# Kernel optimization log

Measured on AMD Instinct MI355X. Metric: run time of the kernel, lower is better.

Reference implementation:

```python
import jax, jax.numpy as jnp
import numpy as np
import math

D = 1024
B, S = 8, 2048


def setup_inputs() -> dict:
    key = jax.random.key(0)
    ks = jax.random.split(key, 8)
    q = jax.random.normal(ks[0], (B, S, D), dtype=jnp.float32)
    k = jax.random.normal(ks[1], (B, S, D), dtype=jnp.float32)
    v1 = jax.random.normal(ks[2], (B, S, D), dtype=jnp.float32)
    mask = jax.random.normal(ks[3], (1, S, S), dtype=jnp.float32)
    # Linear params: torch Linear stores W as [out, in]; init ~ U(-1/sqrt(in), 1/sqrt(in))
    lim = 1.0 / math.sqrt(D)
    W1 = jax.random.uniform(ks[4], (D, D), jnp.float32, -lim, lim)
    b1 = jax.random.uniform(ks[5], (D,), jnp.float32, -lim, lim)
    W2 = jax.random.uniform(ks[6], (D, D), jnp.float32, -lim, lim)
    b2 = jax.random.uniform(ks[7], (D,), jnp.float32, -lim, lim)
    return {"q": q, "k": k, "v1": v1, "mask": mask,
            "W1": W1, "b1": b1, "W2": W2, "b2": b2}


def _proj(x, W1, b1, W2, b2):
    # linear2(linear1(x)); torch Linear: x @ W.T + b
    h = jnp.einsum('bsd,od->bso', x, W1) + b1
    return jnp.einsum('bsd,od->bso', h, W2) + b2


def reference(q, k, v1, mask, W1, b1, W2, b2):
    qp = _proj(q, W1, b1, W2, b2)          # [B,S,D]
    kp = _proj(k, W1, b1, W2, b2)          # [B,S,D]
    scale = 1.0 / math.sqrt(qp.shape[-1])
    qk = jnp.einsum('bqd,bkd->bqk', qp, kp) * scale  # [B,S,S]
    qk = qk + mask                          # broadcast [1,S,S]
    attn = jax.nn.softmax(qk, axis=-1)
    return jnp.einsum('bqk,bkd->bqd', attn, v1)  # [B,S,D]
```

## Files before the change

### kernel.cpp

```cpp
#include <hip/hip_runtime.h>
#include <hip/hip_bf16.h>

typedef __hip_bfloat16 bf16;
typedef __bf16 bf16x8 __attribute__((ext_vector_type(8)));
typedef float f32x4 __attribute__((ext_vector_type(4)));

constexpr int Bn = 8, Sn = 2048, Dn = 1024;
constexpr int BM = 128, BN = 128, BK = 64;

__global__ void cast2_f32_bf16_k(const float* __restrict__ x0, const float* __restrict__ x1,
                                 bf16* __restrict__ y, int n ) {
  int i = (blockIdx.x * blockDim.x + threadIdx.x) * 4;
  const float* src = (i < n) ? (x0 + i) : (x1 + (i - n));
  float4 f = *reinterpret_cast<const float4*>(src);
  bf16 tmp[4] = {__float2bfloat16(f.x), __float2bfloat16(f.y),
                 __float2bfloat16(f.z), __float2bfloat16(f.w)};
  *reinterpret_cast<short4*>(y + i) = *reinterpret_cast<const short4*>(tmp);
}

__global__ void cast_f32_bf16_k(const float* __restrict__ x, bf16* __restrict__ y, int n) {
  int i = (blockIdx.x * blockDim.x + threadIdx.x) * 4;
  if (i >= n) return;
  float4 f = *reinterpret_cast<const float4*>(x + i);
  bf16 tmp[4] = {__float2bfloat16(f.x), __float2bfloat16(f.y),
                 __float2bfloat16(f.z), __float2bfloat16(f.w)};
  *reinterpret_cast<short4*>(y + i) = *reinterpret_cast<const short4*>(tmp);
}

__global__ void transpose_cast_k(const float* __restrict__ src0, bf16* __restrict__ dst0,
                                 int R, int C) {
  __shared__ float tile[32][33];
  const int r0 = blockIdx.x * 32, c0 = blockIdx.y * 32, b = blockIdx.z;
  const float* src = src0 + (size_t)b * R * C;
  bf16* dst = dst0 + (size_t)b * C * R;
  const int tx = threadIdx.x & 31, ty = threadIdx.x >> 5;
  #pragma unroll
  for (int i = 0; i < 4; ++i) {
    int r = ty + i * 8;
    tile[r][tx] = src[(size_t)(r0 + r) * C + c0 + tx];
  }
  __syncthreads();
  #pragma unroll
  for (int i = 0; i < 4; ++i) {
    int c = ty + i * 8;
    dst[(size_t)(c0 + c) * R + r0 + tx] = __float2bfloat16(tile[tx][c]);
  }
}

__global__ __launch_bounds__(256)
void bias_compose_k(const float* __restrict__ W2, const float* __restrict__ b1,
                    const float* __restrict__ b2, float* __restrict__ bc) {
  const int row = blockIdx.x;
  const int t = threadIdx.x;
  float4 wv = *reinterpret_cast<const float4*>(W2 + (size_t)row * Dn + t * 4);
  float4 bv = *reinterpret_cast<const float4*>(b1 + t * 4);
  float s = wv.x * bv.x + wv.y * bv.y + wv.z * bv.z + wv.w * bv.w;
  #pragma unroll
  for (int off = 32; off >= 1; off >>= 1) s += __shfl_xor(s, off);
  __shared__ float ssum[4];
  if ((t & 63) == 0) ssum[t >> 6] = s;
  __syncthreads();
  if (t == 0) bc[row] = (ssum[0] + ssum[1]) + (ssum[2] + ssum[3]) + b2[row];
}

#define SBAR()  asm volatile("s_barrier" ::: "memory")
#define LGKM0() asm volatile("s_waitcnt lgkmcnt(0)" ::: "memory")
#define VM0()   asm volatile("s_waitcnt vmcnt(0)" ::: "memory")

#define MFMA16() do {                                                         \
    __builtin_amdgcn_s_setprio(1);                                            \
    _Pragma("unroll")                                                         \
    for (int kk = 0; kk < 2; ++kk)                                            \
      _Pragma("unroll")                                                       \
      for (int mi4 = 0; mi4 < 4; ++mi4)                                       \
        _Pragma("unroll")                                                     \
        for (int n2 = 0; n2 < 2; ++n2)                                        \
          acc[mi4][n2] = __builtin_amdgcn_mfma_f32_16x16x32_bf16(             \
              aF[mi4][kk], bF[n2][kk], acc[mi4][n2], 0, 0, 0);                \
    __builtin_amdgcn_s_setprio(0);                                            \
  } while (0)

#define ITER(cur, T) do {                                                     \
    const bool pf = (T) + 1 < NT;                                             \
    if (pf) {                                                                 \
      stage2((1 - (cur)) * 32768,         Abase, (T) + 1);                    \
      stage2((1 - (cur)) * 32768 + 16384, Bbase, (T) + 1);                    \
    }                                                                         \
    _Pragma("unroll")                                                         \
    for (int mi4 = 0; mi4 < 4; ++mi4) {                                       \
      aF[mi4][0] = *reinterpret_cast<const bf16x8*>(pA0 + (cur)*32768 + mi4*2048); \
      aF[mi4][1] = *reinterpret_cast<const bf16x8*>(pA1 + (cur)*32768 + mi4*2048); \
    }                                                                         \
    _Pragma("unroll")                                                         \
    for (int j = 0; j < 2; ++j) {                                             \
      bF[j][0] = *reinterpret_cast<const bf16x8*>(pB0 + (cur)*32768 + j*2048); \
      bF[j][1] = *reinterpret_cast<const bf16x8*>(pB1 + (cur)*32768 + j*2048); \
    }                                                                         \
    LGKM0();                                                                  \
    MFMA16();                                                                 \
    if (pf) VM0();                                                            \
    SBAR();                                                                   \
  } while (0)

template<int EPI>
__global__ __launch_bounds__(512, 4)
void gemm128_k(const bf16* __restrict__ A, const bf16* __restrict__ BT,
               void* __restrict__ Cv, const float* __restrict__ aux,
               int N, int K, long long sAz, long long sBz, long long sCz,
               float scale, int gx, int gy)
{
  __shared__ __align__(128) bf16 sh[2 * 16384];

  const int nwg = (int)gridDim.x;
  const int flat = (int)blockIdx.x;
  const int swz = (flat & 7) * (nwg >> 3) + (flat >> 3);
  const int tn = swz % gx;
  const int rem = swz / gx;
  const int tm = rem % gy;
  const int z  = rem / gy;

  const int t = threadIdx.x, w = t >> 6, lane = t & 63;
  const int wm = w >> 2, wn = w & 3;
  const int fr = lane & 15, kg = lane >> 4;
  const int m0 = tm * BM, n0 = tn * BN;
  const bf16* Abase = A + (size_t)z * sAz + (size_t)m0 * K;
  const bf16* Bbase = BT + (size_t)z * sBz + (size_t)n0 * K;

  f32x4 acc[4][2];
  const f32x4 fz = {0.f, 0.f, 0.f, 0.f};
  #pragma unroll
  for (int i = 0; i < 4; ++i) { acc[i][0] = fz; acc[i][1] = fz; }
  bf16x8 aF[4][2], bF[2][2];

  const char* shB = (const char*)sh;
  const int swzlo = (fr & 3) << 4;
  const int swzhi = (fr & 4) << 4;
  const int aoff0 = (wm * 64 + fr) * 128 + ((kg * 16) ^ swzlo) + swzhi;
  const int boff0 = 16384 + (wn * 32 + fr) * 128 + ((kg * 16) ^ swzlo) + swzhi;
  const char* pA0 = shB + aoff0;
  const char* pA1 = shB + (aoff0 ^ 64);
  const char* pB0 = shB + boff0;
  const char* pB1 = shB + (boff0 ^ 64);

  int gOff[2];
  #pragma unroll
  for (int i = 0; i < 2; ++i) {
    const int slot = i * 512 + w * 64 + lane;
    const int row = slot >> 3;
    const int cb = (slot & 7) ^ (row & 7);
    gOff[i] = row * K + cb * 8;
  }
  auto stage2 = [&](int dstByte, const bf16* gbase, int kt) {
    const bf16* g0 = gbase + (size_t)kt * BK;
    char* db = (char*)sh + dstByte;
    #pragma unroll
    for (int i = 0; i < 2; ++i) {
      __builtin_amdgcn_global_load_lds(
          (__attribute__((address_space(1))) void*)(g0 + gOff[i]),
          (__attribute__((address_space(3))) void*)(db + (i * 512 + w * 64) * 16),
          16, 0, 0);
    }
  };

  const int NT = K / BK;
  stage2(0,     Abase, 0);
  stage2(16384, Bbase, 0);
  VM0();
  SBAR();

  for (int T = 0; T < NT; T += 2) {
    ITER(0, T);
    ITER(1, T + 1);
  }

  const int or0 = kg * 4;
  if constexpr (EPI == 0) {
    bf16* C = (bf16*)Cv + (size_t)z * sCz;
    #pragma unroll
    for (int mi = 0; mi < 4; ++mi)
      #pragma unroll
      for (int r = 0; r < 4; ++r) {
        const int row = m0 + wm * 64 + mi * 16 + or0 + r;
        #pragma unroll
        for (int nj = 0; nj < 2; ++nj) {
          const int col = n0 + wn * 32 + nj * 16 + fr;
          C[(size_t)row * N + col] = __float2bfloat16(acc[mi][nj][r] + aux[col]);
        }
      }
  } else if constexpr (EPI == 1) {
    bf16* C = (bf16*)Cv + (size_t)z * sCz;
    #pragma unroll
    for (int mi = 0; mi < 4; ++mi)
      #pragma unroll
      for (int r = 0; r < 4; ++r) {
        const int row = m0 + wm * 64 + mi * 16 + or0 + r;
        #pragma unroll
        for (int nj = 0; nj < 2; ++nj) {
          const int col = n0 + wn * 32 + nj * 16 + fr;
          float v = __expf(acc[mi][nj][r] * scale + aux[(size_t)row * N + col]);
          C[(size_t)row * N + col] = __float2bfloat16(v);
        }
      }
  } else if constexpr (EPI == 2) {
    float* C = (float*)Cv + (size_t)z * sCz;
    const float* Zb = aux + (size_t)z * Sn;
    #pragma unroll
    for (int mi = 0; mi < 4; ++mi)
      #pragma unroll
      for (int r = 0; r < 4; ++r) {
        const int row = m0 + wm * 64 + mi * 16 + or0 + r;
        const float invZ = 1.0f / Zb[row];
        #pragma unroll
        for (int nj = 0; nj < 2; ++nj) {
          const int col = n0 + wn * 32 + nj * 16 + fr;
          C[(size_t)row * N + col] = acc[mi][nj][r] * invZ;
        }
      }
  } else {
    bf16* C = (bf16*)Cv + (size_t)z * sCz;
    #pragma unroll
    for (int mi = 0; mi < 4; ++mi)
      #pragma unroll
      for (int r = 0; r < 4; ++r) {
        const int row = m0 + wm * 64 + mi * 16 + or0 + r;
        #pragma unroll
        for (int nj = 0; nj < 2; ++nj) {
          const int col = n0 + wn * 32 + nj * 16 + fr;
          C[(size_t)row * N + col] = __float2bfloat16(acc[mi][nj][r]);
        }
      }
  }
}

__global__ __launch_bounds__(256)
void rowsum_k(const bf16* __restrict__ sc, float* __restrict__ Z) {
  const size_t row = blockIdx.x;
  const bf16* p = sc + row * (size_t)Sn;
  const int t = threadIdx.x;
  unsigned short raw[8];
  *reinterpret_cast<int4*>(raw) = *reinterpret_cast<const int4*>(p + t * 8);
  float s = 0.f;
  #pragma unroll
  for (int j = 0; j < 8; ++j) s += __uint_as_float(((unsigned)raw[j]) << 16);
  #pragma unroll
  for (int off = 32; off >= 1; off >>= 1) s += __shfl_xor(s, off);
  __shared__ float ssum[4];
  if ((t & 63) == 0) ssum[t >> 6] = s;
  __syncthreads();
  if (t == 0) Z[row] = (ssum[0] + ssum[1]) + (ssum[2] + ssum[3]);
}

extern "C" void kernel_launch(void* const* d_in, const int* in_sizes, int n_in,
                              void* d_out, int out_size, void* d_ws, size_t ws_size,
                              hipStream_t stream) {
  const float* q    = (const float*)d_in[0];
  const float* k    = (const float*)d_in[1];
  const float* v1   = (const float*)d_in[2];
  const float* mask = (const float*)d_in[3];
  const float* W1   = (const float*)d_in[4];
  const float* b1   = (const float*)d_in[5];
  const float* W2   = (const float*)d_in[6];
  const float* b2   = (const float*)d_in[7];
  float* out = (float*)d_out;

  const size_t nQKD = (size_t)Bn * Sn * Dn;
  char* ws = (char*)d_ws;
  bf16* qkb  = (bf16*)ws;
  bf16* vtb  = qkb + 2 * nQKD;
  bf16* hb   = vtb + nQKD;
  bf16* w1t  = hb + 2 * nQKD;
  bf16* w2b  = w1t + (size_t)Dn * Dn;
  bf16* wcb  = w2b + (size_t)Dn * Dn;
  bf16* scb  = wcb + (size_t)Dn * Dn;
  float* Zb  = (float*)(scb + (size_t)Bn * Sn * Sn);
  float* bcb = Zb + (size_t)Bn * Sn;

  dim3 blk(256);
  const int nQK = (int)nQKD;
  cast2_f32_bf16_k<<<dim3(2 * nQK / 4 / 256), blk, 0, stream>>>(q, k, qkb, nQK);
  cast_f32_bf16_k<<<dim3(Dn * Dn / 4 / 256), blk, 0, stream>>>(W2, w2b, Dn * Dn);
  transpose_cast_k<<<dim3(Dn / 32, Dn / 32, 1), blk, 0, stream>>>(W1, w1t, Dn, Dn);
  transpose_cast_k<<<dim3(Sn / 32, Dn / 32, Bn), blk, 0, stream>>>(v1, vtb, Sn, Dn);
  bias_compose_k<<<dim3(Dn), blk, 0, stream>>>(W2, b1, b2, bcb);

  const int M2 = 2 * Bn * Sn;
  dim3 gblk(512);
  gemm128_k<3><<<dim3(8 * 8), gblk, 0, stream>>>(
      w2b, w1t, wcb, nullptr, Dn, Dn, 0, 0, 0, 1.f, 8, 8);
  gemm128_k<0><<<dim3(8 * (M2 / 128)), gblk, 0, stream>>>(
      qkb, wcb, hb, bcb, Dn, Dn, 0, 0, 0, 1.f, 8, M2 / 128);
  gemm128_k<1><<<dim3(16 * 16 * Bn), gblk, 0, stream>>>(
      hb, hb + nQKD, scb, mask, Sn, Dn,
      (long long)Sn * Dn, (long long)Sn * Dn, (long long)Sn * Sn, 0.03125f, 16, 16);
  rowsum_k<<<dim3(Bn * Sn), blk, 0, stream>>>(scb, Zb);
  gemm128_k<2><<<dim3(8 * 16 * Bn), gblk, 0, stream>>>(
      scb, vtb, out, Zb, Dn, Sn,
      (long long)Sn * Sn, (long long)Dn * Sn, (long long)Sn * Dn, 1.f, 8, 16);
}
```

Baseline: 341.3 us.

## Fuse fp32-to-bf16 cast of q/k into projection GEMM A-loads; bf16 mask

Removes the separate cast kernel for q and k. The projection GEMM now loads fp32 A tiles into registers, converts them to bf16 and writes them to LDS itself, which saves one write and read of 2×B×S×D bf16 in global memory. The mask is pre-cast to bf16 once, so the score epilogue reads half the bytes. In exchange, A staging now goes through registers instead of direct global-to-LDS loads, adding register pressure and an extra LDS-write wait per iteration, and the mask loses precision.

```diff
diff --git a/kernel.cpp b/kernel.cpp
--- a/kernel.cpp
+++ b/kernel.cpp
@@ -7,16 +7,6 @@
 
 constexpr int Bn = 8, Sn = 2048, Dn = 1024;
 constexpr int BM = 128, BN = 128, BK = 64;
-
-__global__ void cast2_f32_bf16_k(const float* __restrict__ x0, const float* __restrict__ x1,
-                                 bf16* __restrict__ y, int n ) {
-  int i = (blockIdx.x * blockDim.x + threadIdx.x) * 4;
-  const float* src = (i < n) ? (x0 + i) : (x1 + (i - n));
-  float4 f = *reinterpret_cast<const float4*>(src);
-  bf16 tmp[4] = {__float2bfloat16(f.x), __float2bfloat16(f.y),
-                 __float2bfloat16(f.z), __float2bfloat16(f.w)};
-  *reinterpret_cast<short4*>(y + i) = *reinterpret_cast<const short4*>(tmp);
-}
 
 __global__ void cast_f32_bf16_k(const float* __restrict__ x, bf16* __restrict__ y, int n) {
   int i = (blockIdx.x * blockDim.x + threadIdx.x) * 4;
@@ -82,8 +72,17 @@
 
 #define ITER(cur, T) do {                                                     \
     const bool pf = (T) + 1 < NT;                                             \
+    float4 a0, a1, a2, a3;                                                    \
     if (pf) {                                                                 \
-      stage2((1 - (cur)) * 32768,         Abase, (T) + 1);                    \
+      if constexpr (AF32) {                                                   \
+        const float* gf = Af + (size_t)((T) + 1) * BK;                        \
+        a0 = *reinterpret_cast<const float4*>(gf + gOffF[0]);                 \
+        a1 = *reinterpret_cast<const float4*>(gf + gOffF[0] + 4);             \
+        a2 = *reinterpret_cast<const float4*>(gf + gOffF[1]);                 \
+        a3 = *reinterpret_cast<const float4*>(gf + gOffF[1] + 4);             \
+      } else {                                                                \
+        stage2((1 - (cur)) * 32768, Abase, (T) + 1);                          \
+      }                                                                       \
       stage2((1 - (cur)) * 32768 + 16384, Bbase, (T) + 1);                    \
     }                                                                         \
     _Pragma("unroll")                                                         \
@@ -98,14 +97,22 @@
     }                                                                         \
     LGKM0();                                                                  \
     MFMA16();                                                                 \
-    if (pf) VM0();                                                            \
+    if (pf) {                                                                 \
+      VM0();                                                                  \
+      if constexpr (AF32) {                                                   \
+        wrA((1 - (cur)) * 32768, a0, a1, a2, a3);                             \
+        LGKM0();                                                              \
+      }                                                                       \
+    }                                                                         \
     SBAR();                                                                   \
   } while (0)
 
-template<int EPI>
+template<int EPI, bool AF32>
 __global__ __launch_bounds__(512, 4)
-void gemm128_k(const bf16* __restrict__ A, const bf16* __restrict__ BT,
-               void* __restrict__ Cv, const float* __restrict__ aux,
+void gemm128_k(const bf16* __restrict__ A,
+               const float* __restrict__ Aq, const float* __restrict__ Ak, int rowSplit,
+               const bf16* __restrict__ BT,
+               void* __restrict__ Cv, const void* __restrict__ auxv,
                int N, int K, long long sAz, long long sBz, long long sCz,
                float scale, int gx, int gy)
 {
@@ -125,6 +132,9 @@
   const int m0 = tm * BM, n0 = tn * BN;
   const bf16* Abase = A + (size_t)z * sAz + (size_t)m0 * K;
   const bf16* Bbase = BT + (size_t)z * sBz + (size_t)n0 * K;
+  const float* Af = nullptr;
+  if constexpr (AF32)
+    Af = (m0 < rowSplit) ? Aq + (size_t)m0 * K : Ak + (size_t)(m0 - rowSplit) * K;
 
   f32x4 acc[4][2];
   const f32x4 fz = {0.f, 0.f, 0.f, 0.f};
@@ -142,13 +152,14 @@
   const char* pB0 = shB + boff0;
   const char* pB1 = shB + (boff0 ^ 64);
 
-  int gOff[2];
+  int gOff[2], gOffF[2];
   #pragma unroll
   for (int i = 0; i < 2; ++i) {
     const int slot = i * 512 + w * 64 + lane;
     const int row = slot >> 3;
     const int cb = (slot & 7) ^ (row & 7);
-    gOff[i] = row * K + cb * 8;
+    gOff[i]  = row * K + cb * 8;
+    gOffF[i] = row * K + cb * 8;
   }
   auto stage2 = [&](int dstByte, const bf16* gbase, int kt) {
     const bf16* g0 = gbase + (size_t)kt * BK;
@@ -161,12 +172,31 @@
           16, 0, 0);
     }
   };
+  auto wrA = [&](int dstByte, float4 x0, float4 x1, float4 x2, float4 x3) {
+    char* db = (char*)sh + dstByte;
+    bf16 tmp[16] = {
+      __float2bfloat16(x0.x), __float2bfloat16(x0.y), __float2bfloat16(x0.z), __float2bfloat16(x0.w),
+      __float2bfloat16(x1.x), __float2bfloat16(x1.y), __float2bfloat16(x1.z), __float2bfloat16(x1.w),
+      __float2bfloat16(x2.x), __float2bfloat16(x2.y), __float2bfloat16(x2.z), __float2bfloat16(x2.w),
+      __float2bfloat16(x3.x), __float2bfloat16(x3.y), __float2bfloat16(x3.z), __float2bfloat16(x3.w)};
+    *reinterpret_cast<int4*>(db + (0 * 512 + t) * 16) = *reinterpret_cast<const int4*>(tmp);
+    *reinterpret_cast<int4*>(db + (1 * 512 + t) * 16) = *reinterpret_cast<const int4*>(tmp + 8);
+  };
 
   const int NT = K / BK;
-  stage2(0,     Abase, 0);
-  stage2(16384, Bbase, 0);
-  VM0();
-  SBAR();
+  if constexpr (AF32) {
+    float4 a0 = *reinterpret_cast<const float4*>(Af + gOffF[0]);
+    float4 a1 = *reinterpret_cast<const float4*>(Af + gOffF[0] + 4);
+    float4 a2 = *reinterpret_cast<const float4*>(Af + gOffF[1]);
+    float4 a3 = *reinterpret_cast<const float4*>(Af + gOffF[1] + 4);
+    stage2(16384, Bbase, 0);
+    wrA(0, a0, a1, a2, a3);
+    VM0(); LGKM0(); SBAR();
+  } else {
+    stage2(0,     Abase, 0);
+    stage2(16384, Bbase, 0);
+    VM0(); SBAR();
+  }
 
   for (int T = 0; T < NT; T += 2) {
     ITER(0, T);
@@ -176,6 +206,7 @@
   const int or0 = kg * 4;
   if constexpr (EPI == 0) {
     bf16* C = (bf16*)Cv + (size_t)z * sCz;
+    const float* aux = (const float*)auxv;
     #pragma unroll
     for (int mi = 0; mi < 4; ++mi)
       #pragma unroll
@@ -189,6 +220,7 @@
       }
   } else if constexpr (EPI == 1) {
     bf16* C = (bf16*)Cv + (size_t)z * sCz;
+    const bf16* M = (const bf16*)auxv;
     #pragma unroll
     for (int mi = 0; mi < 4; ++mi)
       #pragma unroll
@@ -197,13 +229,14 @@
         #pragma unroll
         for (int nj = 0; nj < 2; ++nj) {
           const int col = n0 + wn * 32 + nj * 16 + fr;
-          float v = __expf(acc[mi][nj][r] * scale + aux[(size_t)row * N + col]);
+          float mv = __bfloat162float(M[(size_t)row * N + col]);
+          float v = __expf(acc[mi][nj][r] * scale + mv);
           C[(size_t)row * N + col] = __float2bfloat16(v);
         }
       }
   } else if constexpr (EPI == 2) {
     float* C = (float*)Cv + (size_t)z * sCz;
-    const float* Zb = aux + (size_t)z * Sn;
+    const float* Zb = (const float*)auxv + (size_t)z * Sn;
     #pragma unroll
     for (int mi = 0; mi < 4; ++mi)
       #pragma unroll
@@ -265,35 +298,34 @@
 
   const size_t nQKD = (size_t)Bn * Sn * Dn;
   char* ws = (char*)d_ws;
-  bf16* qkb  = (bf16*)ws;
-  bf16* vtb  = qkb + 2 * nQKD;
-  bf16* hb   = vtb + nQKD;
-  bf16* w1t  = hb + 2 * nQKD;
-  bf16* w2b  = w1t + (size_t)Dn * Dn;
-  bf16* wcb  = w2b + (size_t)Dn * Dn;
-  bf16* scb  = wcb + (size_t)Dn * Dn;
-  float* Zb  = (float*)(scb + (size_t)Bn * Sn * Sn);
-  float* bcb = Zb + (size_t)Bn * Sn;
+  bf16* vtb   = (bf16*)ws;
+  bf16* hb    = vtb + nQKD;
+  bf16* w1t   = hb + 2 * nQKD;
+  bf16* w2b   = w1t + (size_t)Dn * Dn;
+  bf16* wcb   = w2b + (size_t)Dn * Dn;
+  bf16* maskb = wcb + (size_t)Dn * Dn;
+  bf16* scb   = maskb + (size_t)Sn * Sn;
+  float* Zb   = (float*)(scb + (size_t)Bn * Sn * Sn);
+  float* bcb  = Zb + (size_t)Bn * Sn;
 
   dim3 blk(256);
-  const int nQK = (int)nQKD;
-  cast2_f32_bf16_k<<<dim3(2 * nQK / 4 / 256), blk, 0, stream>>>(q, k, qkb, nQK);
   cast_f32_bf16_k<<<dim3(Dn * Dn / 4 / 256), blk, 0, stream>>>(W2, w2b, Dn * Dn);
+  cast_f32_bf16_k<<<dim3(Sn * Sn / 4 / 256), blk, 0, stream>>>(mask, maskb, Sn * Sn);
   transpose_cast_k<<<dim3(Dn / 32, Dn / 32, 1), blk, 0, stream>>>(W1, w1t, Dn, Dn);
   transpose_cast_k<<<dim3(Sn / 32, Dn / 32, Bn), blk, 0, stream>>>(v1, vtb, Sn, Dn);
   bias_compose_k<<<dim3(Dn), blk, 0, stream>>>(W2, b1, b2, bcb);
 
   const int M2 = 2 * Bn * Sn;
   dim3 gblk(512);
-  gemm128_k<3><<<dim3(8 * 8), gblk, 0, stream>>>(
-      w2b, w1t, wcb, nullptr, Dn, Dn, 0, 0, 0, 1.f, 8, 8);
-  gemm128_k<0><<<dim3(8 * (M2 / 128)), gblk, 0, stream>>>(
-      qkb, wcb, hb, bcb, Dn, Dn, 0, 0, 0, 1.f, 8, M2 / 128);
-  gemm128_k<1><<<dim3(16 * 16 * Bn), gblk, 0, stream>>>(
-      hb, hb + nQKD, scb, mask, Sn, Dn,
+  gemm128_k<3, false><<<dim3(8 * 8), gblk, 0, stream>>>(
+      w2b, nullptr, nullptr, 0, w1t, wcb, nullptr, Dn, Dn, 0, 0, 0, 1.f, 8, 8);
+  gemm128_k<0, true><<<dim3(8 * (M2 / 128)), gblk, 0, stream>>>(
+      nullptr, q, k, Bn * Sn, wcb, hb, bcb, Dn, Dn, 0, 0, 0, 1.f, 8, M2 / 128);
+  gemm128_k<1, false><<<dim3(16 * 16 * Bn), gblk, 0, stream>>>(
+      hb, nullptr, nullptr, 0, hb + nQKD, scb, maskb, Sn, Dn,
       (long long)Sn * Dn, (long long)Sn * Dn, (long long)Sn * Sn, 0.03125f, 16, 16);
   rowsum_k<<<dim3(Bn * Sn), blk, 0, stream>>>(scb, Zb);
-  gemm128_k<2><<<dim3(8 * 16 * Bn), gblk, 0, stream>>>(
-      scb, vtb, out, Zb, Dn, Sn,
+  gemm128_k<2, false><<<dim3(8 * 16 * Bn), gblk, 0, stream>>>(
+      scb, nullptr, nullptr, 0, vtb, out, Zb, Dn, Sn,
       (long long)Sn * Sn, (long long)Dn * Sn, (long long)Sn * Dn, 1.f, 8, 16);
 }
```

Result: slower. 406.5 us (+19.1%).

## Fold the composed projection into a Gram matrix so only K is projected

Applied to the files above, without the earlier changes.

Rewrites the scores algebraically as q·(Wcᵀ Wc)·kᵀ plus rank-one bias terms. It precomputes the Gram matrix G and the vectors u = Wcᵀbc and c0 = bc·bc, and stops projecting q. Only k goes through the large projection GEMM, and the bias contributions are added in the score epilogue as per-row and per-column scalars. The q/k fp32→bf16 cast is fused with the dot products against u, which adds a few small kernels. The extra bf16 rounding of G and the row-constant term folded into the unshifted exp could shift numerics slightly.

```diff
diff --git a/kernel.cpp b/kernel.cpp
--- a/kernel.cpp
+++ b/kernel.cpp
@@ -7,16 +7,6 @@
 
 constexpr int Bn = 8, Sn = 2048, Dn = 1024;
 constexpr int BM = 128, BN = 128, BK = 64;
-
-__global__ void cast2_f32_bf16_k(const float* __restrict__ x0, const float* __restrict__ x1,
-                                 bf16* __restrict__ y, int n ) {
-  int i = (blockIdx.x * blockDim.x + threadIdx.x) * 4;
-  const float* src = (i < n) ? (x0 + i) : (x1 + (i - n));
-  float4 f = *reinterpret_cast<const float4*>(src);
-  bf16 tmp[4] = {__float2bfloat16(f.x), __float2bfloat16(f.y),
-                 __float2bfloat16(f.z), __float2bfloat16(f.w)};
-  *reinterpret_cast<short4*>(y + i) = *reinterpret_cast<const short4*>(tmp);
-}
 
 __global__ void cast_f32_bf16_k(const float* __restrict__ x, bf16* __restrict__ y, int n) {
   int i = (blockIdx.x * blockDim.x + threadIdx.x) * 4;
@@ -61,6 +51,64 @@
   if ((t & 63) == 0) ssum[t >> 6] = s;
   __syncthreads();
   if (t == 0) bc[row] = (ssum[0] + ssum[1]) + (ssum[2] + ssum[3]) + b2[row];
+}
+
+__global__ __launch_bounds__(256)
+void udot_k(const bf16* __restrict__ wct, const float* __restrict__ bc,
+            float* __restrict__ u) {
+  const int i = blockIdx.x, t = threadIdx.x;
+  short4 wv = *reinterpret_cast<const short4*>(wct + (size_t)i * Dn + t * 4);
+  float4 bv = *reinterpret_cast<const float4*>(bc + t * 4);
+  float s = __uint_as_float(((unsigned)(unsigned short)wv.x) << 16) * bv.x
+          + __uint_as_float(((unsigned)(unsigned short)wv.y) << 16) * bv.y
+          + __uint_as_float(((unsigned)(unsigned short)wv.z) << 16) * bv.z
+          + __uint_as_float(((unsigned)(unsigned short)wv.w) << 16) * bv.w;
+  #pragma unroll
+  for (int off = 32; off >= 1; off >>= 1) s += __shfl_xor(s, off);
+  __shared__ float ssum[4];
+  if ((t & 63) == 0) ssum[t >> 6] = s;
+  __syncthreads();
+  if (t == 0) u[i] = (ssum[0] + ssum[1]) + (ssum[2] + ssum[3]);
+}
+
+__global__ __launch_bounds__(256)
+void c0_k(const float* __restrict__ bc, float* __restrict__ c0) {
+  const int t = threadIdx.x;
+  float4 bv = *reinterpret_cast<const float4*>(bc + t * 4);
+  float s = bv.x * bv.x + bv.y * bv.y + bv.z * bv.z + bv.w * bv.w;
+  #pragma unroll
+  for (int off = 32; off >= 1; off >>= 1) s += __shfl_xor(s, off);
+  __shared__ float ssum[4];
+  if ((t & 63) == 0) ssum[t >> 6] = s;
+  __syncthreads();
+  if (t == 0) c0[0] = (ssum[0] + ssum[1]) + (ssum[2] + ssum[3]);
+}
+
+__global__ __launch_bounds__(256)
+void castdot_k(const float* __restrict__ q, const float* __restrict__ k,
+               const float* __restrict__ u, const float* __restrict__ c0,
+               bf16* __restrict__ dst, float* __restrict__ qu, float* __restrict__ ku) {
+  const int row = blockIdx.x;
+  const bool isQ = row < Bn * Sn;
+  const float* src = isQ ? q + (size_t)row * Dn : k + (size_t)(row - Bn * Sn) * Dn;
+  const int t = threadIdx.x;
+  float4 f = *reinterpret_cast<const float4*>(src + t * 4);
+  bf16 tmp[4] = {__float2bfloat16(f.x), __float2bfloat16(f.y),
+                 __float2bfloat16(f.z), __float2bfloat16(f.w)};
+  *reinterpret_cast<short4*>(dst + (size_t)row * Dn + t * 4) =
+      *reinterpret_cast<const short4*>(tmp);
+  float4 uv = *reinterpret_cast<const float4*>(u + t * 4);
+  float s = f.x * uv.x + f.y * uv.y + f.z * uv.z + f.w * uv.w;
+  #pragma unroll
+  for (int off = 32; off >= 1; off >>= 1) s += __shfl_xor(s, off);
+  __shared__ float ssum[4];
+  if ((t & 63) == 0) ssum[t >> 6] = s;
+  __syncthreads();
+  if (t == 0) {
+    float tot = (ssum[0] + ssum[1]) + (ssum[2] + ssum[3]);
+    if (isQ) qu[row] = tot + c0[0];
+    else     ku[row - Bn * Sn] = tot;
+  }
 }
 
 #define SBAR()  asm volatile("s_barrier" ::: "memory")
@@ -105,7 +153,8 @@
 template<int EPI>
 __global__ __launch_bounds__(512, 4)
 void gemm128_k(const bf16* __restrict__ A, const bf16* __restrict__ BT,
-               void* __restrict__ Cv, const float* __restrict__ aux,
+               void* __restrict__ Cv, const void* __restrict__ auxv,
+               const float* __restrict__ qu, const float* __restrict__ ku,
                int N, int K, long long sAz, long long sBz, long long sCz,
                float scale, int gx, int gy)
 {
@@ -174,36 +223,28 @@
   }
 
   const int or0 = kg * 4;
-  if constexpr (EPI == 0) {
+  if constexpr (EPI == 1) {
     bf16* C = (bf16*)Cv + (size_t)z * sCz;
+    const float* M = (const float*)auxv;
+    const float* quz = qu + (size_t)z * Sn;
+    const float* kuz = ku + (size_t)z * Sn;
     #pragma unroll
     for (int mi = 0; mi < 4; ++mi)
       #pragma unroll
       for (int r = 0; r < 4; ++r) {
         const int row = m0 + wm * 64 + mi * 16 + or0 + r;
+        const float quv = quz[row];
         #pragma unroll
         for (int nj = 0; nj < 2; ++nj) {
           const int col = n0 + wn * 32 + nj * 16 + fr;
-          C[(size_t)row * N + col] = __float2bfloat16(acc[mi][nj][r] + aux[col]);
-        }
-      }
-  } else if constexpr (EPI == 1) {
-    bf16* C = (bf16*)Cv + (size_t)z * sCz;
-    #pragma unroll
-    for (int mi = 0; mi < 4; ++mi)
-      #pragma unroll
-      for (int r = 0; r < 4; ++r) {
-        const int row = m0 + wm * 64 + mi * 16 + or0 + r;
-        #pragma unroll
-        for (int nj = 0; nj < 2; ++nj) {
-          const int col = n0 + wn * 32 + nj * 16 + fr;
-          float v = __expf(acc[mi][nj][r] * scale + aux[(size_t)row * N + col]);
+          float v = __expf((acc[mi][nj][r] + quv + kuz[col]) * scale
+                           + M[(size_t)row * N + col]);
           C[(size_t)row * N + col] = __float2bfloat16(v);
         }
       }
   } else if constexpr (EPI == 2) {
     float* C = (float*)Cv + (size_t)z * sCz;
-    const float* Zb = aux + (size_t)z * Sn;
+    const float* Zb = (const float*)auxv + (size_t)z * Sn;
     #pragma unroll
     for (int mi = 0; mi < 4; ++mi)
       #pragma unroll
@@ -218,6 +259,7 @@
       }
   } else {
     bf16* C = (bf16*)Cv + (size_t)z * sCz;
+    bf16* CT = (EPI == 4) ? (bf16*)const_cast<void*>(auxv) : nullptr;
     #pragma unroll
     for (int mi = 0; mi < 4; ++mi)
       #pragma unroll
@@ -226,7 +268,9 @@
         #pragma unroll
         for (int nj = 0; nj < 2; ++nj) {
           const int col = n0 + wn * 32 + nj * 16 + fr;
-          C[(size_t)row * N + col] = __float2bfloat16(acc[mi][nj][r]);
+          const bf16 v = __float2bfloat16(acc[mi][nj][r]);
+          C[(size_t)row * N + col] = v;
+          if constexpr (EPI == 4) CT[(size_t)col * N + row] = v;
         }
       }
   }
@@ -264,36 +308,45 @@
   float* out = (float*)d_out;
 
   const size_t nQKD = (size_t)Bn * Sn * Dn;
+  const size_t nDD = (size_t)Dn * Dn;
   char* ws = (char*)d_ws;
-  bf16* qkb  = (bf16*)ws;
-  bf16* vtb  = qkb + 2 * nQKD;
-  bf16* hb   = vtb + nQKD;
-  bf16* w1t  = hb + 2 * nQKD;
-  bf16* w2b  = w1t + (size_t)Dn * Dn;
-  bf16* wcb  = w2b + (size_t)Dn * Dn;
-  bf16* scb  = wcb + (size_t)Dn * Dn;
+  bf16* vtb  = (bf16*)ws;
+  bf16* qkb  = vtb + nQKD;
+  bf16* kgb  = qkb + 2 * nQKD;
+  bf16* w1t  = kgb + nQKD;
+  bf16* w2b  = w1t + nDD;
+  bf16* wcb  = w2b + nDD;
+  bf16* wct  = wcb + nDD;
+  bf16* gb   = wct + nDD;
+  bf16* scb  = gb + nDD;
   float* Zb  = (float*)(scb + (size_t)Bn * Sn * Sn);
-  float* bcb = Zb + (size_t)Bn * Sn;
+  float* qub = Zb + (size_t)Bn * Sn;
+  float* kub = qub + (size_t)Bn * Sn;
+  float* bcb = kub + (size_t)Bn * Sn;
+  float* ub  = bcb + Dn;
+  float* c0v = ub + Dn;
 
   dim3 blk(256);
-  const int nQK = (int)nQKD;
-  cast2_f32_bf16_k<<<dim3(2 * nQK / 4 / 256), blk, 0, stream>>>(q, k, qkb, nQK);
   cast_f32_bf16_k<<<dim3(Dn * Dn / 4 / 256), blk, 0, stream>>>(W2, w2b, Dn * Dn);
   transpose_cast_k<<<dim3(Dn / 32, Dn / 32, 1), blk, 0, stream>>>(W1, w1t, Dn, Dn);
   transpose_cast_k<<<dim3(Sn / 32, Dn / 32, Bn), blk, 0, stream>>>(v1, vtb, Sn, Dn);
   bias_compose_k<<<dim3(Dn), blk, 0, stream>>>(W2, b1, b2, bcb);
 
-  const int M2 = 2 * Bn * Sn;
   dim3 gblk(512);
+  gemm128_k<4><<<dim3(8 * 8), gblk, 0, stream>>>(
+      w2b, w1t, wcb, wct, nullptr, nullptr, Dn, Dn, 0, 0, 0, 1.f, 8, 8);
   gemm128_k<3><<<dim3(8 * 8), gblk, 0, stream>>>(
-      w2b, w1t, wcb, nullptr, Dn, Dn, 0, 0, 0, 1.f, 8, 8);
-  gemm128_k<0><<<dim3(8 * (M2 / 128)), gblk, 0, stream>>>(
-      qkb, wcb, hb, bcb, Dn, Dn, 0, 0, 0, 1.f, 8, M2 / 128);
+      wct, wct, gb, nullptr, nullptr, nullptr, Dn, Dn, 0, 0, 0, 1.f, 8, 8);
+  udot_k<<<dim3(Dn), blk, 0, stream>>>(wct, bcb, ub);
+  c0_k<<<dim3(1), blk, 0, stream>>>(bcb, c0v);
+  castdot_k<<<dim3(2 * Bn * Sn), blk, 0, stream>>>(q, k, ub, c0v, qkb, qub, kub);
+  gemm128_k<3><<<dim3(8 * 128), gblk, 0, stream>>>(
+      qkb + nQKD, gb, kgb, nullptr, nullptr, nullptr, Dn, Dn, 0, 0, 0, 1.f, 8, 128);
   gemm128_k<1><<<dim3(16 * 16 * Bn), gblk, 0, stream>>>(
-      hb, hb + nQKD, scb, mask, Sn, Dn,
+      qkb, kgb, scb, mask, qub, kub, Sn, Dn,
       (long long)Sn * Dn, (long long)Sn * Dn, (long long)Sn * Sn, 0.03125f, 16, 16);
   rowsum_k<<<dim3(Bn * Sn), blk, 0, stream>>>(scb, Zb);
   gemm128_k<2><<<dim3(8 * 16 * Bn), gblk, 0, stream>>>(
-      scb, vtb, out, Zb, Dn, Sn,
+      scb, vtb, out, Zb, nullptr, nullptr, Dn, Sn,
       (long long)Sn * Sn, (long long)Dn * Sn, (long long)Sn * Dn, 1.f, 8, 16);
 }
```

Measured after the change: 322.2 us (median of 3 runs). 5.6% less time.
